# Performance work log

Hardware: AMD Instinct MI355X
Metric: run time of the kernel (lower is better)

## Reference

```python
import jax, jax.numpy as jnp
import numpy as np

N_NODES = 4096
N_EDGES = 262144
D = 128
N_REL = 1000
N_ENT = 50000


def setup_inputs() -> dict:
    key = jax.random.key(0)
    ks = jax.random.split(key, 6)
    x = jax.random.normal(ks[0], (N_NODES, D), dtype=jnp.float32)
    edge_index = jax.random.randint(ks[1], (2, N_EDGES), 0, N_NODES)
    relation_id = jax.random.randint(ks[2], (N_EDGES,), 0, N_REL)
    neg_flag = jax.random.randint(ks[3], (N_EDGES,), 0, 2)
    rel_emb = jax.random.normal(ks[4], (N_REL, D), dtype=jnp.float32)
    entity_emb = jax.random.normal(ks[5], (N_ENT, D), dtype=jnp.float32)
    scale = jnp.ones((N_ENT,), dtype=jnp.float32)
    bias = jnp.zeros((N_ENT,), dtype=jnp.float32)
    return {"x": x, "edge_index": edge_index, "relation_id": relation_id,
            "neg_flag": neg_flag, "rel_emb": rel_emb, "entity_emb": entity_emb,
            "scale": scale, "bias": bias}


def reference(x, edge_index, relation_id, neg_flag, rel_emb, entity_emb, scale, bias):
    src, dst = edge_index[0], edge_index[1]
    # message: gather x_j, TransE tail estimate, sign flip for negated atoms
    neg_coef = 1.0 - 2.0 * neg_flag.astype(x.dtype)           # [E]
    msg = (x[src] + rel_emb[relation_id]) * neg_coef[:, None]  # [E, D]
    # aggregate: scatter-add into target nodes
    aggr_out = jax.ops.segment_sum(msg, dst, num_segments=x.shape[0])  # [N, D]
    # update: residual + bias/scale double-matmul through entity table
    aggr = 0.1 * x + aggr_out                                  # [N, D]
    entity_score = aggr @ entity_emb.T                          # [N, V]
    entity_score = jax.nn.relu(entity_score * scale + bias)
    out = entity_score @ entity_emb                             # [N, D]
    return out
```

## Files before the change

kernel.cpp:

```cpp
#include <hip/hip_runtime.h>
#include <stdint.h>

typedef __attribute__((ext_vector_type(8))) short short8;
typedef __attribute__((ext_vector_type(8))) unsigned short ushort8;
typedef __attribute__((ext_vector_type(4))) float f32x4;
typedef __attribute__((ext_vector_type(16))) float f32x16;
typedef __attribute__((ext_vector_type(2))) unsigned int uint2v;

#define NNODES 4096
#define NEDGES 262144
#define DIM 128
#define NENT 50000
#define NENTP 50048
#define NTILES 782
#define NSPLIT 16
#define CHUNK 49

__device__ __forceinline__ unsigned short f2bf(float f) {
  union { __bf16 b; unsigned short u; } c;
  c.b = (__bf16)f;
  return c.u;
}

__global__ __launch_bounds__(256) void k_hist(
    const int* __restrict__ ei, int* __restrict__ cnt)
{
  int e = blockIdx.x * 256 + threadIdx.x;
  atomicAdd(&cnt[ei[NEDGES + e]], 1);
}

__global__ __launch_bounds__(1024) void k_scan(
    const int* __restrict__ cnt, int* __restrict__ off, int* __restrict__ cur)
{
  __shared__ int s[1024];
  int t = threadIdx.x;
  int4 v = reinterpret_cast<const int4*>(cnt)[t];
  int lsum = v.x + v.y + v.z + v.w;
  s[t] = lsum; __syncthreads();
  for (int d = 1; d < 1024; d <<= 1) {
    int a = (t >= d) ? s[t - d] : 0;
    __syncthreads();
    s[t] += a;
    __syncthreads();
  }
  int base = s[t] - lsum;
  int4 o; o.x = base; o.y = base + v.x; o.z = o.y + v.y; o.w = o.z + v.z;
  reinterpret_cast<int4*>(off)[t] = o;
  reinterpret_cast<int4*>(cur)[t] = o;
  if (t == 1023) off[4096] = base + lsum;
}

__global__ __launch_bounds__(256) void k_place(
    const int* __restrict__ ei, const int* __restrict__ rid,
    const int* __restrict__ nf, int* __restrict__ cur, int* __restrict__ sorted)
{
  int e = blockIdx.x * 256 + threadIdx.x;
  int dst = ei[NEDGES + e];
  int pos = atomicAdd(&cur[dst], 1);
  sorted[pos] = ei[e] | (rid[e] << 12) | (nf[e] << 22);
}

__global__ __launch_bounds__(256) void k_aggr(
    const int* __restrict__ off, const int* __restrict__ sorted,
    const float* __restrict__ x, const float* __restrict__ rel,
    unsigned short* __restrict__ q)
{
  __shared__ float sAcc[8 * 132];
  const int n = blockIdx.x;
  const int t = threadIdx.x;
  const int slot = t >> 5;
  const int c = t & 31;
  const int b = off[n], eN = off[n + 1];
  float4 acc = make_float4(0.f, 0.f, 0.f, 0.f);
  for (int i = b + slot; i < eN; i += 8) {
    int p = sorted[i];
    float4 xv = reinterpret_cast<const float4*>(x)[(p & 4095) * 32 + c];
    float4 rv = reinterpret_cast<const float4*>(rel)[((p >> 12) & 1023) * 32 + c];
    float sgn = (p & (1 << 22)) ? -1.f : 1.f;
    acc.x += sgn * (xv.x + rv.x);
    acc.y += sgn * (xv.y + rv.y);
    acc.z += sgn * (xv.z + rv.z);
    acc.w += sgn * (xv.w + rv.w);
  }
  *reinterpret_cast<float4*>(&sAcc[slot * 132 + c * 4]) = acc;
  __syncthreads();
  if (t < 128) {
    float s = 0.f;
#pragma unroll
    for (int k = 0; k < 8; ++k) s += sAcc[k * 132 + t];
    q[n * DIM + t] = f2bf(0.1f * x[n * DIM + t] + s);
  }
}

__global__ __launch_bounds__(256) void k_prep(
    const float* __restrict__ ent, const float* __restrict__ scale,
    unsigned short* __restrict__ ebf, unsigned short* __restrict__ etbf)
{
  __shared__ float sT[64 * 133];
  const int t = threadIdx.x;
  const int e0 = blockIdx.x * 64;
#pragma unroll
  for (int i = 0; i < 8; ++i) {
    int idx = i * 256 + t;
    int e = idx >> 5;
    int c4 = idx & 31;
    float4 v = make_float4(0.f, 0.f, 0.f, 0.f);
    float sc = 0.f;
    if (e0 + e < NENT) {
      v = reinterpret_cast<const float4*>(ent)[(e0 + e) * 32 + c4];
      sc = scale[e0 + e];
    }
    *reinterpret_cast<float4*>(&sT[e * 133 + c4 * 4]) = v;
    ushort4 bq;
    bq.x = f2bf(v.x * sc); bq.y = f2bf(v.y * sc);
    bq.z = f2bf(v.z * sc); bq.w = f2bf(v.w * sc);
    *reinterpret_cast<ushort4*>(&ebf[(e0 + e) * 128 + c4 * 4]) = bq;
  }
  __syncthreads();
  const int lane = t & 63;
  const int w = t >> 6;
  const int dl = lane >> 3;
  const int el = (lane & 7) * 8;
#pragma unroll
  for (int it = 0; it < 4; ++it) {
    int d = it * 32 + w * 8 + dl;
    ushort8 buf;
#pragma unroll
    for (int j = 0; j < 8; ++j) buf[j] = f2bf(sT[(el + j) * 133 + d]);
    *reinterpret_cast<ushort8*>(&etbf[d * NENTP + e0 + el]) = buf;
  }
}


__device__ __forceinline__ void gll16(const void* g, void* l) {
  __builtin_amdgcn_global_load_lds(
      (const __attribute__((address_space(1))) unsigned int*)g,
      (__attribute__((address_space(3))) unsigned int*)l, 16, 0, 0);
}

__device__ __forceinline__ unsigned cvtpk(float lo, float hi) {
  unsigned r;
  asm("v_cvt_pk_bf16_f32 %0, %1, %2" : "=v"(r) : "v"(lo), "v"(hi));
  return r;
}

__global__ __launch_bounds__(256, 2) void k_flash(
    const unsigned short* __restrict__ qg,
    const unsigned short* __restrict__ ebf,
    const unsigned short* __restrict__ etbf,
    const float* __restrict__ bias,
    float* __restrict__ out)
{
  __shared__ __align__(16) unsigned short sE[2][64 * 128];
  __shared__ __align__(16) unsigned short sET[2][128 * 64];
  __shared__ __align__(16) float sBias[2][64];

  const int t = threadIdx.x;
  const int w = t >> 6;
  const int lane = t & 63;
  const int l31 = lane & 31;
  const int hi = lane >> 5;

  const int m0 = blockIdx.x * 128;
  const int tile_lo = blockIdx.y * CHUNK;
  const int tile_hi = (tile_lo + CHUNK < NTILES) ? (tile_lo + CHUNK) : NTILES;

  const int cE = (((t & 15) ^ ((t >> 4) & 15))) * 8;
  const int rE = (t >> 4) & 15;
  const int cT = (((t & 7) ^ ((t >> 3) & 7))) * 8;
  const int rT = t >> 3;

  short8 qf[8];
  {
    const unsigned short* qrow = qg + (size_t)(m0 + w * 32 + l31) * DIM + hi * 8;
#pragma unroll
    for (int kk = 0; kk < 8; ++kk)
      qf[kk] = *reinterpret_cast<const short8*>(qrow + kk * 16);
  }

  f32x16 accO[4];
#pragma unroll
  for (int td = 0; td < 4; ++td)
#pragma unroll
    for (int r = 0; r < 16; ++r) accO[td][r] = 0.f;

  {
    const int vt = tile_lo * 64;
#pragma unroll
    for (int i = 0; i < 4; ++i)
      gll16(ebf + (size_t)(vt + i * 16 + rE) * DIM + cE, &sE[0][i * 2048 + w * 512]);
#pragma unroll
    for (int i = 0; i < 4; ++i)
      gll16(etbf + (size_t)(i * 32 + rT) * NENTP + vt + cT, &sET[0][i * 2048 + w * 512]);
    if (t < 64) sBias[0][t] = (vt + t < NENT) ? bias[vt + t] : 0.f;
  }
  __syncthreads();

  int cur = 0;
  for (int tile = tile_lo; tile < tile_hi; ++tile) {
    if (tile + 1 < tile_hi) {
      const int vt = (tile + 1) * 64;
#pragma unroll
      for (int i = 0; i < 4; ++i)
        gll16(ebf + (size_t)(vt + i * 16 + rE) * DIM + cE, &sE[cur ^ 1][i * 2048 + w * 512]);
#pragma unroll
      for (int i = 0; i < 4; ++i)
        gll16(etbf + (size_t)(i * 32 + rT) * NENTP + vt + cT, &sET[cur ^ 1][i * 2048 + w * 512]);
      if (t < 64) sBias[cur ^ 1][t] = (vt + t < NENT) ? bias[vt + t] : 0.f;
    }

    f32x16 accST[2];
#pragma unroll
    for (int te = 0; te < 2; ++te)
#pragma unroll
      for (int r = 0; r < 16; ++r) accST[te][r] = 0.f;

    const unsigned short* sEc = sE[cur];
    __builtin_amdgcn_s_setprio(1);
#pragma unroll
    for (int kk = 0; kk < 8; ++kk) {
      const int col = ((kk * 2 + hi) ^ (l31 & 15)) * 8;
      short8 a0 = *reinterpret_cast<const short8*>(&sEc[l31 * 128 + col]);
      short8 a1 = *reinterpret_cast<const short8*>(&sEc[(32 + l31) * 128 + col]);
      accST[0] = __builtin_amdgcn_mfma_f32_32x32x16_bf16(a0, qf[kk], accST[0], 0, 0, 0);
      accST[1] = __builtin_amdgcn_mfma_f32_32x32x16_bf16(a1, qf[kk], accST[1], 0, 0, 0);
    }
    __builtin_amdgcn_s_setprio(0);

    short8 F[4];
    const float* sb = sBias[cur];
#pragma unroll
    for (int te = 0; te < 2; ++te) {
      float p[16];
#pragma unroll
      for (int g = 0; g < 4; ++g) {
        f32x4 b4 = *reinterpret_cast<const f32x4*>(&sb[te * 32 + g * 8 + hi * 4]);
#pragma unroll
        for (int j = 0; j < 4; ++j)
          p[g * 4 + j] = fmaxf(accST[te][g * 4 + j] + b4[j], 0.f);
      }
      unsigned wr[8];
#pragma unroll
      for (int c2 = 0; c2 < 8; ++c2) wr[c2] = cvtpk(p[2 * c2], p[2 * c2 + 1]);
      uint2v r02 = __builtin_amdgcn_permlane32_swap(wr[0], wr[2], false, false);
      uint2v r13 = __builtin_amdgcn_permlane32_swap(wr[1], wr[3], false, false);
      uint2v r46 = __builtin_amdgcn_permlane32_swap(wr[4], wr[6], false, false);
      uint2v r57 = __builtin_amdgcn_permlane32_swap(wr[5], wr[7], false, false);
      union { unsigned u[4]; short8 s; } f0, f1;
      f0.u[0] = r02[0]; f0.u[1] = r13[0]; f0.u[2] = r02[1]; f0.u[3] = r13[1];
      f1.u[0] = r46[0]; f1.u[1] = r57[0]; f1.u[2] = r46[1]; f1.u[3] = r57[1];
      F[te * 2 + 0] = f0.s;
      F[te * 2 + 1] = f1.s;
    }

    const unsigned short* sTc = sET[cur];
    __builtin_amdgcn_s_setprio(1);
#pragma unroll
    for (int ke = 0; ke < 4; ++ke) {
#pragma unroll
      for (int td = 0; td < 4; ++td) {
        const int d = td * 32 + l31;
        const int col = ((ke * 2 + hi) ^ (l31 & 7)) * 8;
        short8 bT = *reinterpret_cast<const short8*>(&sTc[d * 64 + col]);
        accO[td] = __builtin_amdgcn_mfma_f32_32x32x16_bf16(F[ke], bT, accO[td], 0, 0, 0);
      }
    }
    __builtin_amdgcn_s_setprio(0);

    __syncthreads();
    cur ^= 1;
  }

#pragma unroll
  for (int td = 0; td < 4; ++td) {
#pragma unroll
    for (int r = 0; r < 16; ++r) {
      int qrow = (r & 3) + 8 * (r >> 2) + 4 * hi;
      int row = m0 + w * 32 + qrow;
      int col = td * 32 + l31;
      atomicAdd(&out[(size_t)row * DIM + col], accO[td][r]);
    }
  }
}

extern "C" void kernel_launch(void* const* d_in, const int* in_sizes, int n_in,
                              void* d_out, int out_size, void* d_ws, size_t ws_size,
                              hipStream_t stream) {
  const float* x     = (const float*)d_in[0];
  const int*   ei    = (const int*)d_in[1];
  const int*   rid   = (const int*)d_in[2];
  const int*   nf    = (const int*)d_in[3];
  const float* rel   = (const float*)d_in[4];
  const float* ent   = (const float*)d_in[5];
  const float* scale = (const float*)d_in[6];
  const float* bias  = (const float*)d_in[7];
  float* out = (float*)d_out;

  char* ws = (char*)d_ws;
  int*            cnt    = (int*)(ws + 0);
  int*            off    = (int*)(ws + (16u << 10));
  int*            cur    = (int*)(ws + (36u << 10));
  int*            sorted = (int*)(ws + (64u << 10));
  unsigned short* qb     = (unsigned short*)(ws + (1344u << 10));
  unsigned short* ebf    = (unsigned short*)(ws + (2560u << 10));
  unsigned short* etbf   = (unsigned short*)(ws + (2560u << 10) + (size_t)NENTP * DIM * 2);

  hipMemsetAsync(cnt, 0, 4096 * sizeof(int), stream);
  hipMemsetAsync(d_out, 0, (size_t)out_size * sizeof(float), stream);
  k_prep<<<NTILES, 256, 0, stream>>>(ent, scale, ebf, etbf);
  k_hist<<<NEDGES / 256, 256, 0, stream>>>(ei, cnt);
  k_scan<<<1, 1024, 0, stream>>>(cnt, off, cur);
  k_place<<<NEDGES / 256, 256, 0, stream>>>(ei, rid, nf, cur, sorted);
  k_aggr<<<NNODES, 256, 0, stream>>>(off, sorted, x, rel, qb);
  k_flash<<<dim3(NNODES / 128, NSPLIT), 256, 0, stream>>>(qb, ebf, etbf, bias, out);
}
```

Baseline: 276.4 us.

## Double rows per block in flash kernel to reuse entity tiles across two query tiles

Each wave now handles 64 query rows (two 32-row tiles) instead of 32, so every entity tile loaded into LDS and every B-fragment read is reused for twice as many MFMAs. The grid becomes 16 row blocks by 32 entity splits (512 blocks, as before), with balanced split boundaries. This halves global/LDS traffic per FLOP but doubles accumulator registers (accO becomes 128 floats plus Q fragments), which risks spills or lower occupancy under launch_bounds(256,2).

```diff
diff --git a/kernel.cpp b/kernel.cpp
--- a/kernel.cpp
+++ b/kernel.cpp
@@ -13,8 +13,7 @@
 #define NENT 50000
 #define NENTP 50048
 #define NTILES 782
-#define NSPLIT 16
-#define CHUNK 49
+#define NSPLIT 32
 
 __device__ __forceinline__ unsigned short f2bf(float f) {
   union { __bf16 b; unsigned short u; } c;
@@ -161,28 +160,32 @@
   const int l31 = lane & 31;
   const int hi = lane >> 5;
 
-  const int m0 = blockIdx.x * 128;
-  const int tile_lo = blockIdx.y * CHUNK;
-  const int tile_hi = (tile_lo + CHUNK < NTILES) ? (tile_lo + CHUNK) : NTILES;
+  const int m0 = blockIdx.x * 256;
+  const int tile_lo = (blockIdx.y * NTILES) / NSPLIT;
+  const int tile_hi = ((blockIdx.y + 1) * NTILES) / NSPLIT;
 
   const int cE = (((t & 15) ^ ((t >> 4) & 15))) * 8;
   const int rE = (t >> 4) & 15;
   const int cT = (((t & 7) ^ ((t >> 3) & 7))) * 8;
   const int rT = t >> 3;
 
-  short8 qf[8];
-  {
-    const unsigned short* qrow = qg + (size_t)(m0 + w * 32 + l31) * DIM + hi * 8;
+  short8 qf[2][8];
+#pragma unroll
+  for (int tq = 0; tq < 2; ++tq) {
+    const unsigned short* qrow =
+        qg + (size_t)(m0 + w * 64 + tq * 32 + l31) * DIM + hi * 8;
 #pragma unroll
     for (int kk = 0; kk < 8; ++kk)
-      qf[kk] = *reinterpret_cast<const short8*>(qrow + kk * 16);
-  }
-
-  f32x16 accO[4];
-#pragma unroll
-  for (int td = 0; td < 4; ++td)
-#pragma unroll
-    for (int r = 0; r < 16; ++r) accO[td][r] = 0.f;
+      qf[tq][kk] = *reinterpret_cast<const short8*>(qrow + kk * 16);
+  }
+
+  f32x16 accO[2][4];
+#pragma unroll
+  for (int tq = 0; tq < 2; ++tq)
+#pragma unroll
+    for (int td = 0; td < 4; ++td)
+#pragma unroll
+      for (int r = 0; r < 16; ++r) accO[tq][td][r] = 0.f;
 
   {
     const int vt = tile_lo * 64;
@@ -209,48 +212,51 @@
       if (t < 64) sBias[cur ^ 1][t] = (vt + t < NENT) ? bias[vt + t] : 0.f;
     }
 
-    f32x16 accST[2];
-#pragma unroll
-    for (int te = 0; te < 2; ++te)
-#pragma unroll
-      for (int r = 0; r < 16; ++r) accST[te][r] = 0.f;
-
     const unsigned short* sEc = sE[cur];
-    __builtin_amdgcn_s_setprio(1);
-#pragma unroll
-    for (int kk = 0; kk < 8; ++kk) {
-      const int col = ((kk * 2 + hi) ^ (l31 & 15)) * 8;
-      short8 a0 = *reinterpret_cast<const short8*>(&sEc[l31 * 128 + col]);
-      short8 a1 = *reinterpret_cast<const short8*>(&sEc[(32 + l31) * 128 + col]);
-      accST[0] = __builtin_amdgcn_mfma_f32_32x32x16_bf16(a0, qf[kk], accST[0], 0, 0, 0);
-      accST[1] = __builtin_amdgcn_mfma_f32_32x32x16_bf16(a1, qf[kk], accST[1], 0, 0, 0);
-    }
-    __builtin_amdgcn_s_setprio(0);
-
-    short8 F[4];
     const float* sb = sBias[cur];
+    short8 F[2][4];
 #pragma unroll
     for (int te = 0; te < 2; ++te) {
-      float p[16];
-#pragma unroll
-      for (int g = 0; g < 4; ++g) {
-        f32x4 b4 = *reinterpret_cast<const f32x4*>(&sb[te * 32 + g * 8 + hi * 4]);
-#pragma unroll
-        for (int j = 0; j < 4; ++j)
-          p[g * 4 + j] = fmaxf(accST[te][g * 4 + j] + b4[j], 0.f);
+      f32x16 accST[2];
+#pragma unroll
+      for (int tq = 0; tq < 2; ++tq)
+#pragma unroll
+        for (int r = 0; r < 16; ++r) accST[tq][r] = 0.f;
+
+      __builtin_amdgcn_s_setprio(1);
+#pragma unroll
+      for (int kk = 0; kk < 8; ++kk) {
+        const int col = ((kk * 2 + hi) ^ (l31 & 15)) * 8;
+        short8 a = *reinterpret_cast<const short8*>(
+            &sEc[(te * 32 + l31) * 128 + col]);
+        accST[0] = __builtin_amdgcn_mfma_f32_32x32x16_bf16(a, qf[0][kk], accST[0], 0, 0, 0);
+        accST[1] = __builtin_amdgcn_mfma_f32_32x32x16_bf16(a, qf[1][kk], accST[1], 0, 0, 0);
       }
-      unsigned wr[8];
-#pragma unroll
-      for (int c2 = 0; c2 < 8; ++c2) wr[c2] = cvtpk(p[2 * c2], p[2 * c2 + 1]);
-      uint2v r02 = __builtin_amdgcn_permlane32_swap(wr[0], wr[2], false, false);
-      uint2v r13 = __builtin_amdgcn_permlane32_swap(wr[1], wr[3], false, false);
-      uint2v r46 = __builtin_amdgcn_permlane32_swap(wr[4], wr[6], false, false);
-      uint2v r57 = __builtin_amdgcn_permlane32_swap(wr[5], wr[7], false, false);
-      union { unsigned u[4]; short8 s; } f0, f1;
-      f0.u[0] = r02[0]; f0.u[1] = r13[0]; f0.u[2] = r02[1]; f0.u[3] = r13[1];
-      f1.u[0] = r46[0]; f1.u[1] = r57[0]; f1.u[2] = r46[1]; f1.u[3] = r57[1];
-      F[te * 2 + 0] = f0.s;
-      F[te * 2 + 1] = f1.s;
+      __builtin_amdgcn_s_setprio(0);
+
+#pragma unroll
+      for (int tq = 0; tq < 2; ++tq) {
+        float p[16];
+#pragma unroll
+        for (int g = 0; g < 4; ++g) {
+          f32x4 b4 = *reinterpret_cast<const f32x4*>(&sb[te * 32 + g * 8 + hi * 4]);
+#pragma unroll
+          for (int j = 0; j < 4; ++j)
+            p[g * 4 + j] = fmaxf(accST[tq][g * 4 + j] + b4[j], 0.f);
+        }
+        unsigned wr[8];
+#pragma unroll
+        for (int c2 = 0; c2 < 8; ++c2) wr[c2] = cvtpk(p[2 * c2], p[2 * c2 + 1]);
+        uint2v r02 = __builtin_amdgcn_permlane32_swap(wr[0], wr[2], false, false);
+        uint2v r13 = __builtin_amdgcn_permlane32_swap(wr[1], wr[3], false, false);
+        uint2v r46 = __builtin_amdgcn_permlane32_swap(wr[4], wr[6], false, false);
+        uint2v r57 = __builtin_amdgcn_permlane32_swap(wr[5], wr[7], false, false);
+        union { unsigned u[4]; short8 s; } f0, f1;
+        f0.u[0] = r02[0]; f0.u[1] = r13[0]; f0.u[2] = r02[1]; f0.u[3] = r13[1];
+        f1.u[0] = r46[0]; f1.u[1] = r57[0]; f1.u[2] = r46[1]; f1.u[3] = r57[1];
+        F[tq][te * 2 + 0] = f0.s;
+        F[tq][te * 2 + 1] = f1.s;
+      }
     }
 
     const unsigned short* sTc = sET[cur];
@@ -262,7 +268,8 @@
         const int d = td * 32 + l31;
         const int col = ((ke * 2 + hi) ^ (l31 & 7)) * 8;
         short8 bT = *reinterpret_cast<const short8*>(&sTc[d * 64 + col]);
-        accO[td] = __builtin_amdgcn_mfma_f32_32x32x16_bf16(F[ke], bT, accO[td], 0, 0, 0);
+        accO[0][td] = __builtin_amdgcn_mfma_f32_32x32x16_bf16(F[0][ke], bT, accO[0][td], 0, 0, 0);
+        accO[1][td] = __builtin_amdgcn_mfma_f32_32x32x16_bf16(F[1][ke], bT, accO[1][td], 0, 0, 0);
       }
     }
     __builtin_amdgcn_s_setprio(0);
@@ -272,13 +279,16 @@
   }
 
 #pragma unroll
-  for (int td = 0; td < 4; ++td) {
-#pragma unroll
-    for (int r = 0; r < 16; ++r) {
-      int qrow = (r & 3) + 8 * (r >> 2) + 4 * hi;
-      int row = m0 + w * 32 + qrow;
-      int col = td * 32 + l31;
-      atomicAdd(&out[(size_t)row * DIM + col], accO[td][r]);
+  for (int tq = 0; tq < 2; ++tq) {
+#pragma unroll
+    for (int td = 0; td < 4; ++td) {
+#pragma unroll
+      for (int r = 0; r < 16; ++r) {
+        int qrow = (r & 3) + 8 * (r >> 2) + 4 * hi;
+        int row = m0 + w * 64 + tq * 32 + qrow;
+        int col = td * 32 + l31;
+        atomicAdd(&out[(size_t)row * DIM + col], accO[tq][td][r]);
+      }
     }
   }
 }
@@ -312,5 +322,5 @@
   k_scan<<<1, 1024, 0, stream>>>(cnt, off, cur);
   k_place<<<NEDGES / 256, 256, 0, stream>>>(ei, rid, nf, cur, sorted);
   k_aggr<<<NNODES, 256, 0, stream>>>(off, sorted, x, rel, qb);
-  k_flash<<<dim3(NNODES / 128, NSPLIT), 256, 0, stream>>>(qb, ebf, etbf, bias, out);
-}
+  k_flash<<<dim3(NNODES / 256, NSPLIT), 256, 0, stream>>>(qb, ebf, etbf, bias, out);
+}
```

Measured after the change: 465.0 us. +68.3%, slower.
